# Optimization experiments

Hardware: AMD Instinct MI355X
Metric: run time of the kernel (lower is better)

The kernel has to match this reference:

```python
import jax, jax.numpy as jnp
from jax import lax
import numpy as np

B, H, W, CH, N = 32, 112, 112, 96, 5


def setup_inputs() -> dict:
    key = jax.random.key(0)
    k1, k2 = jax.random.split(key)
    x = jax.random.normal(k1, (B, H, W, CH), dtype=jnp.float32)
    kernel = jax.random.normal(k2, (N, N, CH), dtype=jnp.float32)  # channels_last (kr, kc, ch)
    alpha = jnp.ones((1, 1), dtype=jnp.float32)
    bias = jnp.ones((1, 1), dtype=jnp.float32)
    return {"x": x, "kernel": kernel, "alpha": alpha, "bias": bias}


def reference(x, kernel, alpha, bias):
    # Depthwise SAME conv (zero-padded by n//2, matching K.spatial_2d_padding),
    # per-channel kernel; then affine (alpha, bias), elementwise gate, residual.
    ch = x.shape[-1]
    rhs = kernel[:, :, None, :]  # HWIO: (n, n, 1, ch), feature_group_count=ch
    conv = lax.conv_general_dilated(
        x, rhs,
        window_strides=(1, 1),
        padding="SAME",
        dimension_numbers=("NHWC", "HWIO", "NHWC"),
        feature_group_count=ch,
    )
    gate = conv * alpha[0, 0] + bias[0, 0]
    return gate * x + x
```

## Files before the change

### kernel.cpp

```cpp
#include <hip/hip_runtime.h>
#include <stdint.h>


typedef float f4 __attribute__((ext_vector_type(4)));

#define CHN   96
#define C4    24
#define WI    112
#define HI    112
#define BATCH 32
#define NSPLIT 3
#define CHUNK_ROWS 38
#define ROW   (WI * CHN)
#define IMG   ((size_t)HI * ROW)
#define NTHR  192
#define NBLK  (BATCH * NSPLIT * WI * C4 / NTHR)
#define BPX   (NBLK / 8)

#define SLOTS  3
#define SLOT4  (5 * 64)
#define WAVE4  (SLOTS * SLOT4)
#define NWAVES 3

__device__ __forceinline__ void dma16(const float* g, f4* l) {
    __builtin_amdgcn_global_load_lds(
        (const __attribute__((address_space(1))) uint32_t*)g,
        (__attribute__((address_space(3))) uint32_t*)l,
        16, 0, 0);
}

__device__ __forceinline__ void fma4(f4& a, const f4 t, const f4 v) {
    a.x = fmaf(t.x, v.x, a.x);
    a.y = fmaf(t.y, v.y, a.y);
    a.z = fmaf(t.z, v.z, a.z);
    a.w = fmaf(t.w, v.w, a.w);
}

__global__ __launch_bounds__(NTHR, 2) void dwconv_gate_dma4(
    const float* __restrict__ x,
    const float* __restrict__ kern,
    const float* __restrict__ alpha,
    const float* __restrict__ bias,
    float* __restrict__ out)
{
    __shared__ f4 smem[NWAVES * WAVE4];

    const int tid  = threadIdx.x;
    const int lane = tid & 63;
    const int wave = tid >> 6;
    f4* swave = &smem[wave * WAVE4];

    const int bid = (blockIdx.x & 7) * BPX + (blockIdx.x >> 3);

    const int gid = bid * NTHR + tid;
    const int c4    = gid % C4;
    const int rest  = gid / C4;
    const int w     = rest % WI;
    const int r2    = rest / WI;
    const int chunk = r2 % NSPLIT;
    const int b     = r2 / NSPLIT;

    const float av = alpha[0];
    const float bv = bias[0];
    const f4 z4 = {0.f, 0.f, 0.f, 0.f};

    int toff[5];
#pragma unroll
    for (int dx = 0; dx < 5; ++dx) {
        const int ww = w + dx - 2;
        const int wc = ww < 0 ? 0 : (ww >= WI ? WI - 1 : ww);
        toff[dx] = (wc - w) * CHN;
    }
    f4 wt[25];
#pragma unroll
    for (int i = 0; i < 25; ++i) {
        const int ww = w + (i % 5) - 2;
        wt[i] = ((ww >= 0) && (ww < WI))
              ? *(const f4*)(kern + i * CHN + 4 * c4) : z4;
    }

    const int h0   = chunk * CHUNK_ROWS;
    const int rows = (chunk == NSPLIT - 1) ? (HI - h0) : CHUNK_ROWS;
    const int nit  = rows + 4;

    const float* px = x   + (size_t)b * IMG + (size_t)w * CHN + 4 * c4;
    float*       po = out + (size_t)b * IMG + (size_t)w * CHN + 4 * c4;

#define ISSUE(SLOT, RIN) do {                                              \
        const int _q  = (RIN);                                             \
        const int _qc = _q < 0 ? 0 : (_q >= HI ? HI - 1 : _q);             \
        const float* _g = px + (size_t)_qc * ROW;                          \
        dma16(_g + toff[0], swave + (SLOT) * SLOT4);                       \
        dma16(_g + toff[1], swave + (SLOT) * SLOT4 + 64);                  \
        dma16(_g + toff[2], swave + (SLOT) * SLOT4 + 128);                 \
        dma16(_g + toff[3], swave + (SLOT) * SLOT4 + 192);                 \
        dma16(_g + toff[4], swave + (SLOT) * SLOT4 + 256);                 \
    } while (0)

    ISSUE(0, h0 - 2);
    ISSUE(1, h0 - 1);
    ISSUE(2, h0);

    f4 acc[5] = {z4, z4, z4, z4, z4};
    f4 xp1 = z4, xp2 = z4;

#define BODY(I, SLOT, VMC) do {                                            \
        const int _i = (I);                                                \
        asm volatile("s_waitcnt vmcnt(" #VMC ")" ::: "memory");            \
        const int _rin = h0 - 2 + _i;                                      \
        const bool _rok = (_rin >= 0) && (_rin < HI);   \
        f4 t0, t1, t2, t3, t4;                                             \
        if (_rok) {                                                        \
            const f4* _s = swave + (SLOT) * SLOT4 + lane;                  \
            t0 = _s[0];   t1 = _s[64];  t2 = _s[128];                      \
            t3 = _s[192]; t4 = _s[256];                                    \
        } else {                                                           \
            t0 = z4; t1 = z4; t2 = z4; t3 = z4; t4 = z4;                   \
        }                                                                  \
        _Pragma("unroll")                                                  \
        for (int j = 0; j < 5; ++j) {                                      \
            const int wb = (4 - j) * 5;                                    \
            fma4(acc[j], t0, wt[wb + 0]);                                  \
            fma4(acc[j], t1, wt[wb + 1]);                                  \
            fma4(acc[j], t2, wt[wb + 2]);                                  \
            fma4(acc[j], t3, wt[wb + 3]);                                  \
            fma4(acc[j], t4, wt[wb + 4]);                                  \
        }                                                                  \
        if (_i >= 4) {                                                     \
            f4 o;                                                          \
            o.x = fmaf(fmaf(acc[0].x, av, bv), xp2.x, xp2.x);              \
            o.y = fmaf(fmaf(acc[0].y, av, bv), xp2.y, xp2.y);              \
            o.z = fmaf(fmaf(acc[0].z, av, bv), xp2.z, xp2.z);              \
            o.w = fmaf(fmaf(acc[0].w, av, bv), xp2.w, xp2.w);              \
            __builtin_nontemporal_store(                                   \
                o, (f4*)(po + (ptrdiff_t)(h0 - 4 + _i) * ROW));            \
        }                                                                  \
        xp2 = xp1; xp1 = t2;                                               \
        acc[0] = acc[1]; acc[1] = acc[2]; acc[2] = acc[3];                 \
        acc[3] = acc[4]; acc[4] = z4;                                      \
        ISSUE(SLOT, h0 + 1 + _i);                                          \
    } while (0)

    BODY(0, 0, 10);
    BODY(1, 1, 10);
    BODY(2, 2, 10);
    BODY(3, 0, 10);
    BODY(4, 1, 10);
    BODY(5, 2, 11);

    int i = 6;
    for (; i + 3 <= nit; i += 3) {
        BODY(i + 0, 0, 12);
        BODY(i + 1, 1, 12);
        BODY(i + 2, 2, 12);
    }
    if (i < nit) BODY(i, 0, 12);
#undef BODY
#undef ISSUE
}

extern "C" void kernel_launch(void* const* d_in, const int* in_sizes, int n_in,
                              void* d_out, int out_size, void* d_ws, size_t ws_size,
                              hipStream_t stream) {
    const float* x     = (const float*)d_in[0];
    const float* kern  = (const float*)d_in[1];
    const float* alpha = (const float*)d_in[2];
    const float* bias  = (const float*)d_in[3];
    float* out = (float*)d_out;

    dim3 block(NTHR);
    dim3 grid(NBLK);
    hipLaunchKernelGGL(dwconv_gate_dma4, grid, block, 0, stream,
                       x, kern, alpha, bias, out);
}
```

Measured before the change: 62.26 us.

## Load shared halo tiles cooperatively per wave instead of per-thread five-column loads

Each wave now covers an 8-column by 8-float4-channel patch. It loads one shared 12-column halo row into LDS with two async DMA loads per lane, where before each lane issued five loads for its own neighbours. Threads then read their five horizontal taps from LDS at fixed strides, which cuts redundant global and L2 load traffic and DMA instruction count. The height split doubles to six chunks and the ring buffer grows to four slots with adjusted waitcnt values. The cost is more vertical halo re-reads per chunk and some duplicated lanes in the second load.

Result: faster. 54.31 us (-12.8%).

```diff
diff --git a/kernel.cpp b/kernel.cpp
--- a/kernel.cpp
+++ b/kernel.cpp
@@ -5,20 +5,20 @@
 typedef float f4 __attribute__((ext_vector_type(4)));
 
 #define CHN   96
-#define C4    24
 #define WI    112
 #define HI    112
 #define BATCH 32
-#define NSPLIT 3
-#define CHUNK_ROWS 38
+#define NSPLIT 6
+#define CHUNK_ROWS 19
 #define ROW   (WI * CHN)
 #define IMG   ((size_t)HI * ROW)
 #define NTHR  192
-#define NBLK  (BATCH * NSPLIT * WI * C4 / NTHR)
+#define NWG   14
+#define NBLK  (BATCH * NSPLIT * NWG)
 #define BPX   (NBLK / 8)
 
-#define SLOTS  3
-#define SLOT4  (5 * 64)
+#define SLOTS  4
+#define SLOT4  128
 #define WAVE4  (SLOTS * SLOT4)
 #define NWAVES 3
 
@@ -36,7 +36,7 @@
     a.w = fmaf(t.w, v.w, a.w);
 }
 
-__global__ __launch_bounds__(NTHR, 2) void dwconv_gate_dma4(
+__global__ __launch_bounds__(NTHR, 2) void dwconv_gate_coop(
     const float* __restrict__ x,
     const float* __restrict__ kern,
     const float* __restrict__ alpha,
@@ -45,32 +45,27 @@
 {
     __shared__ f4 smem[NWAVES * WAVE4];
 
-    const int tid  = threadIdx.x;
-    const int lane = tid & 63;
-    const int wave = tid >> 6;
+    const int tid   = threadIdx.x;
+    const int lane  = tid & 63;
+    const int wave  = tid >> 6;
+    const int c4sub = lane & 7;
+    const int wsub  = lane >> 3;
     f4* swave = &smem[wave * WAVE4];
 
     const int bid = (blockIdx.x & 7) * BPX + (blockIdx.x >> 3);
 
-    const int gid = bid * NTHR + tid;
-    const int c4    = gid % C4;
-    const int rest  = gid / C4;
-    const int w     = rest % WI;
-    const int r2    = rest / WI;
-    const int chunk = r2 % NSPLIT;
-    const int b     = r2 / NSPLIT;
+    const int wg    = bid % NWG;
+    const int chunk = (bid / NWG) % NSPLIT;
+    const int b     = bid / (NWG * NSPLIT);
+
+    const int w0 = wg * 8;
+    const int w  = w0 + wsub;
+    const int c4 = wave * 8 + c4sub;
 
     const float av = alpha[0];
     const float bv = bias[0];
     const f4 z4 = {0.f, 0.f, 0.f, 0.f};
 
-    int toff[5];
-#pragma unroll
-    for (int dx = 0; dx < 5; ++dx) {
-        const int ww = w + dx - 2;
-        const int wc = ww < 0 ? 0 : (ww >= WI ? WI - 1 : ww);
-        toff[dx] = (wc - w) * CHN;
-    }
     f4 wt[25];
 #pragma unroll
     for (int i = 0; i < 25; ++i) {
@@ -83,48 +78,57 @@
     const int rows = (chunk == NSPLIT - 1) ? (HI - h0) : CHUNK_ROWS;
     const int nit  = rows + 4;
 
-    const float* px = x   + (size_t)b * IMG + (size_t)w * CHN + 4 * c4;
+    const float* gx = x   + (size_t)b * IMG;
     float*       po = out + (size_t)b * IMG + (size_t)w * CHN + 4 * c4;
+
+    const int t1 = lane;
+    const int t2 = 64 + (lane < 32 ? lane : 31);
+    const int w1 = w0 - 2 + (t1 >> 3);
+    const int w2 = w0 - 2 + (t2 >> 3);
+    const int w1c = w1 < 0 ? 0 : (w1 >= WI ? WI - 1 : w1);
+    const int w2c = w2 < 0 ? 0 : (w2 >= WI ? WI - 1 : w2);
+    const int coff1 = w1c * CHN + 4 * (wave * 8 + (t1 & 7));
+    const int coff2 = w2c * CHN + 4 * (wave * 8 + (t2 & 7));
 
 #define ISSUE(SLOT, RIN) do {                                              \
         const int _q  = (RIN);                                             \
         const int _qc = _q < 0 ? 0 : (_q >= HI ? HI - 1 : _q);             \
-        const float* _g = px + (size_t)_qc * ROW;                          \
-        dma16(_g + toff[0], swave + (SLOT) * SLOT4);                       \
-        dma16(_g + toff[1], swave + (SLOT) * SLOT4 + 64);                  \
-        dma16(_g + toff[2], swave + (SLOT) * SLOT4 + 128);                 \
-        dma16(_g + toff[3], swave + (SLOT) * SLOT4 + 192);                 \
-        dma16(_g + toff[4], swave + (SLOT) * SLOT4 + 256);                 \
+        const float* _r = gx + (size_t)_qc * ROW;                          \
+        dma16(_r + coff1, swave + (SLOT) * SLOT4);                         \
+        dma16(_r + coff2, swave + (SLOT) * SLOT4 + 64);                    \
     } while (0)
 
     ISSUE(0, h0 - 2);
     ISSUE(1, h0 - 1);
     ISSUE(2, h0);
+    ISSUE(3, h0 + 1);
 
     f4 acc[5] = {z4, z4, z4, z4, z4};
     f4 xp1 = z4, xp2 = z4;
+
+    const int rbase = wsub * 8 + c4sub;
 
 #define BODY(I, SLOT, VMC) do {                                            \
         const int _i = (I);                                                \
         asm volatile("s_waitcnt vmcnt(" #VMC ")" ::: "memory");            \
         const int _rin = h0 - 2 + _i;                                      \
         const bool _rok = (_rin >= 0) && (_rin < HI);   \
-        f4 t0, t1, t2, t3, t4;                                             \
+        f4 t0, t1v, t2v, t3, t4;                                           \
         if (_rok) {                                                        \
-            const f4* _s = swave + (SLOT) * SLOT4 + lane;                  \
-            t0 = _s[0];   t1 = _s[64];  t2 = _s[128];                      \
-            t3 = _s[192]; t4 = _s[256];                                    \
+            const f4* _s = swave + (SLOT) * SLOT4 + rbase;                 \
+            t0  = _s[0];  t1v = _s[8];  t2v = _s[16];                      \
+            t3  = _s[24]; t4  = _s[32];                                    \
         } else {                                                           \
-            t0 = z4; t1 = z4; t2 = z4; t3 = z4; t4 = z4;                   \
+            t0 = z4; t1v = z4; t2v = z4; t3 = z4; t4 = z4;                 \
         }                                                                  \
         _Pragma("unroll")                                                  \
         for (int j = 0; j < 5; ++j) {                                      \
             const int wb = (4 - j) * 5;                                    \
-            fma4(acc[j], t0, wt[wb + 0]);                                  \
-            fma4(acc[j], t1, wt[wb + 1]);                                  \
-            fma4(acc[j], t2, wt[wb + 2]);                                  \
-            fma4(acc[j], t3, wt[wb + 3]);                                  \
-            fma4(acc[j], t4, wt[wb + 4]);                                  \
+            fma4(acc[j], t0,  wt[wb + 0]);                                 \
+            fma4(acc[j], t1v, wt[wb + 1]);                                 \
+            fma4(acc[j], t2v, wt[wb + 2]);                                 \
+            fma4(acc[j], t3,  wt[wb + 3]);                                 \
+            fma4(acc[j], t4,  wt[wb + 4]);                                 \
         }                                                                  \
         if (_i >= 4) {                                                     \
             f4 o;                                                          \
@@ -135,26 +139,30 @@
             __builtin_nontemporal_store(                                   \
                 o, (f4*)(po + (ptrdiff_t)(h0 - 4 + _i) * ROW));            \
         }                                                                  \
-        xp2 = xp1; xp1 = t2;                                               \
+        xp2 = xp1; xp1 = t2v;                                              \
         acc[0] = acc[1]; acc[1] = acc[2]; acc[2] = acc[3];                 \
         acc[3] = acc[4]; acc[4] = z4;                                      \
-        ISSUE(SLOT, h0 + 1 + _i);                                          \
+        ISSUE(SLOT, h0 + 2 + _i);                                          \
     } while (0)
 
-    BODY(0, 0, 10);
-    BODY(1, 1, 10);
-    BODY(2, 2, 10);
-    BODY(3, 0, 10);
-    BODY(4, 1, 10);
-    BODY(5, 2, 11);
+    BODY(0, 0, 6);
+    BODY(1, 1, 6);
+    BODY(2, 2, 6);
+    BODY(3, 3, 6);
+    BODY(4, 0, 6);
+    BODY(5, 1, 7);
+    BODY(6, 2, 8);
 
-    int i = 6;
-    for (; i + 3 <= nit; i += 3) {
-        BODY(i + 0, 0, 12);
-        BODY(i + 1, 1, 12);
-        BODY(i + 2, 2, 12);
+    int i = 7;
+    for (; i + 4 <= nit; i += 4) {
+        BODY(i + 0, 3, 9);
+        BODY(i + 1, 0, 9);
+        BODY(i + 2, 1, 9);
+        BODY(i + 3, 2, 9);
     }
-    if (i < nit) BODY(i, 0, 12);
+    for (; i < nit; ++i) {
+        BODY(i, (i & 3) == 0 ? 0 : ((i & 3) == 1 ? 1 : ((i & 3) == 2 ? 2 : 3)), 9);
+    }
 #undef BODY
 #undef ISSUE
 }
@@ -170,6 +178,6 @@
 
     dim3 block(NTHR);
     dim3 grid(NBLK);
-    hipLaunchKernelGGL(dwconv_gate_dma4, grid, block, 0, stream,
+    hipLaunchKernelGGL(dwconv_gate_coop, grid, block, 0, stream,
                        x, kern, alpha, bias, out);
 }
```
